# Kernel tuning notes

Measured on AMD Instinct MI355X. Metric: run time of the kernel, lower is better.

The kernel has to match this reference:

```python
import jax, jax.numpy as jnp
import numpy as np

NUM_HEADS = 16


def setup_inputs() -> dict:
    key = jax.random.key(0)
    k1, k2, k3 = jax.random.split(key, 3)
    x = jax.random.normal(k1, (2, 2048, 1024), dtype=jnp.float32)
    w_qkv = jax.random.normal(k2, (3072, 1024), dtype=jnp.float32) * 0.02
    b_qkv = jax.random.normal(k3, (3072,), dtype=jnp.float32) * 0.02
    return {"x": x, "w_qkv": w_qkv, "b_qkv": b_qkv}


def reference(x, w_qkv, b_qkv):
    b, s, _ = x.shape
    d_model = w_qkv.shape[0] // 3
    head_dim = d_model // NUM_HEADS
    # fused QKV projection (torch Linear: x @ W^T + b)
    qkv = x @ w_qkv.T + b_qkv                      # [b, s, 3*d_model]
    qkv = qkv.reshape(b, s, NUM_HEADS, 3 * head_dim)
    qkv = jnp.transpose(qkv, (0, 2, 1, 3))          # [b, h, s, 3*hd]
    q, k, v = jnp.split(qkv, 3, axis=-1)            # each [b, h, s, hd]
    scale = 1.0 / np.sqrt(head_dim).astype(np.float32)
    scores = jnp.einsum("bhqd,bhkd->bhqk", q, k) * scale
    attn = jax.nn.softmax(scores, axis=-1)
    values = jnp.einsum("bhqk,bhkd->bhqd", attn, v)  # [b, h, s, hd]
    # Faithful to source: reshape WITHOUT permuting heads back (head-interleaved)
    return values.reshape(b, s, d_model)
```

## Files before the change

### kernel.cpp

```cpp
#include <hip/hip_runtime.h>
#include <cstdint>

typedef unsigned short ushort_t;

#define M_ROWS 4096
#define N_COLS 3072
#define K_DIM  1024
#define S_LEN  2048
#define NHEADS 16
#define HDIM   64
#define QSCALE 0.1803368801111204f

typedef __bf16 bf16_t;
typedef bf16_t  bf16x8  __attribute__((ext_vector_type(8)));
typedef short   shortx4 __attribute__((ext_vector_type(4)));
typedef float   floatx4 __attribute__((ext_vector_type(4)));
typedef ushort_t ushortx4 __attribute__((ext_vector_type(4)));

union U32x2S4 { unsigned u[2]; shortx4 s; };

__device__ __forceinline__ unsigned short f2bf(float f) {
  unsigned u = __float_as_uint(f);
  u += 0x7FFFu + ((u >> 16) & 1u);
  return (unsigned short)(u >> 16);
}

__device__ __forceinline__ unsigned pkbf(float a, float b) {
  unsigned ua = __float_as_uint(a) + 0x8000u;
  unsigned ub = __float_as_uint(b) + 0x8000u;
  return __builtin_amdgcn_perm(ub, ua, 0x07060302u);
}

__device__ __forceinline__ unsigned cvtpk(float a, float b) {
#if __has_builtin(__builtin_amdgcn_cvt_pk_bf16_f32)
  auto t = __builtin_amdgcn_cvt_pk_bf16_f32(a, b);
  unsigned r;
  __builtin_memcpy(&r, &t, 4);
  return r;
#else
  return pkbf(a, b);
#endif
}

__device__ __forceinline__ float fexp2(float x) {
#if __has_builtin(__builtin_amdgcn_exp2f)
  return __builtin_amdgcn_exp2f(x);
#else
  float r; asm volatile("v_exp_f32 %0, %1\n\ts_nop 1" : "=v"(r) : "v"(x)); return r;
#endif
}

__device__ __forceinline__ void gload_lds16(const void* g, void* l) {
  __builtin_amdgcn_global_load_lds(
      (const __attribute__((address_space(1))) unsigned int*)g,
      (__attribute__((address_space(3))) unsigned int*)l,
      16, 0, 0);
}

__global__ __launch_bounds__(256) void cvt_bf16_kernel(
    const float* __restrict__ x, const float* __restrict__ w,
    ushort_t* __restrict__ Xb, ushort_t* __restrict__ Wb) {
  const int NX8 = (M_ROWS * K_DIM) / 8;
  int i = blockIdx.x * 256 + threadIdx.x;
  const float4* src;
  ushort_t* dst;
  int idx;
  if (i < NX8) { src = (const float4*)x; dst = Xb; idx = i; }
  else         { src = (const float4*)w; dst = Wb; idx = i - NX8; }
  float4 a = src[2 * idx];
  float4 b = src[2 * idx + 1];
  uint4 o;
  o.x = cvtpk(a.x, a.y);
  o.y = cvtpk(a.z, a.w);
  o.z = cvtpk(b.x, b.y);
  o.w = cvtpk(b.z, b.w);
  *(uint4*)(dst + 8 * (size_t)idx) = o;
}

__global__ __launch_bounds__(256) void qkv_gemm_kernel(
    const ushort_t* __restrict__ Xb, const ushort_t* __restrict__ Wb,
    const float* __restrict__ bias,
    ushort_t* __restrict__ Qb, ushort_t* __restrict__ Kb, ushort_t* __restrict__ Vb) {
  __shared__ ushort_t As[128 * 64];
  __shared__ ushort_t Bs[128 * 64];
  const int tid = threadIdx.x;
  const int l = tid & 63, w = tid >> 6;
  const int quad = l >> 4, lj = l & 15;
  const int m0 = blockIdx.y * 128, n0 = blockIdx.x * 128;
  const int wm = (w & 1) * 64, wn = (w >> 1) * 64;

  floatx4 acc[4][4] = {};

  const int srow = w * 32 + (l >> 3);
  const int scol = ((l & 7) ^ (l >> 3)) * 8;
  const ushort_t* gA = Xb + (size_t)(m0 + srow) * K_DIM + scol;
  const ushort_t* gB = Wb + (size_t)(n0 + srow) * K_DIM + scol;
  ushort_t* lA = As + (w * 32) * 64;
  ushort_t* lB = Bs + (w * 32) * 64;

  const int swr = lj & 7;

  for (int k0 = 0; k0 < K_DIM; k0 += 64) {
    __syncthreads();
#pragma unroll
    for (int c = 0; c < 4; ++c) {
      gload_lds16(gA + (size_t)(c * 8) * K_DIM + k0, lA + c * 8 * 64);
      gload_lds16(gB + (size_t)(c * 8) * K_DIM + k0, lB + c * 8 * 64);
    }
    __syncthreads();
#pragma unroll
    for (int kk = 0; kk < 2; ++kk) {
      const int ch = ((kk * 4 + quad) ^ swr) * 8;
      bf16x8 aF[4], bF[4];
#pragma unroll
      for (int i = 0; i < 4; ++i)
        aF[i] = *(const bf16x8*)(As + (wm + i * 16 + lj) * 64 + ch);
#pragma unroll
      for (int j = 0; j < 4; ++j)
        bF[j] = *(const bf16x8*)(Bs + (wn + j * 16 + lj) * 64 + ch);
#pragma unroll
      for (int i = 0; i < 4; ++i)
#pragma unroll
        for (int j = 0; j < 4; ++j)
          acc[i][j] = __builtin_amdgcn_mfma_f32_16x16x32_bf16(aF[i], bF[j], acc[i][j], 0, 0, 0);
    }
  }

#pragma unroll
  for (int j = 0; j < 4; ++j) {
    const int n = n0 + wn + j * 16 + lj;
    const int h = n / 192;
    const int r = n - h * 192;
    const int seg = r >> 6;
    const int d = r & 63;
    const float bv = bias[n];
    ushort_t* dst = (seg == 0) ? Qb : (seg == 1) ? Kb : Vb;
    const float scl = (seg == 0) ? QSCALE : 1.0f;
    const size_t base = (size_t)h * S_LEN * HDIM + d;
#pragma unroll
    for (int i = 0; i < 4; ++i) {
#pragma unroll
      for (int rg = 0; rg < 4; ++rg) {
        const int m = m0 + wm + i * 16 + quad * 4 + rg;
        const int bi = m >> 11;
        const int si = m & 2047;
        dst[base + ((size_t)bi * NHEADS * S_LEN + si) * HDIM] =
            f2bf((acc[i][j][rg] + bv) * scl);
      }
    }
  }
}

__global__ __launch_bounds__(512, 4) void attn_kernel(
    const ushort_t* __restrict__ Qb, const ushort_t* __restrict__ Kb,
    const ushort_t* __restrict__ Vb, float* __restrict__ out) {
  __shared__ ushort_t Ks[128 * 64];
  __shared__ ushort_t Vs[64 * 140];
  const int tid = threadIdx.x;
  const int l = tid & 63, w = tid >> 6;
  const int quad = l >> 4, lj = l & 15;
  const int bh = blockIdx.x >> 4;
  const int qt = blockIdx.x & 15;
  const int q0 = qt * 128 + w * 16;
  const size_t headoff = (size_t)bh * S_LEN * HDIM;

  bf16x8 qF[2];
#pragma unroll
  for (int kk = 0; kk < 2; ++kk)
    qF[kk] = *(const bf16x8*)(Qb + headoff + (size_t)(q0 + lj) * HDIM +
                              kk * 32 + quad * 8);

  floatx4 accO[4] = {};
  float l_runA = 0.f, l_runB = 0.f;

  const int kr = tid >> 3;
  const int kc = ((tid & 7) ^ (kr & 7)) * 8;
  const ushort_t* gK = Kb + headoff + (size_t)kr * HDIM + kc;
  ushort_t* lK = Ks + tid * 8;

  const int dq = tid & 15;
  const int spw = tid >> 4;
  const ushort_t* gV = Vb + headoff + dq * 4;
  unsigned* Vs32 = (unsigned*)Vs;
  const int swz = (dq >> 2) << 1;

  const int swk = lj & 7;

  for (int kb = 0; kb < 16; ++kb) {
    const int kv0 = kb * 128;
    __syncthreads();
#pragma unroll
    for (int c = 0; c < 2; ++c)
      gload_lds16(gK + (size_t)(kv0 + c * 64) * HDIM, lK + c * 64 * 64);
#pragma unroll
    for (int R = 0; R < 2; ++R) {
      const int sp = R * 32 + spw;
      const ushort_t* g = gV + (size_t)(kv0 + 2 * sp) * HDIM;
      const uint2 v0 = *(const uint2*)g;
      const uint2 v1 = *(const uint2*)(g + HDIM);
      unsigned o0 = __builtin_amdgcn_perm(v1.x, v0.x, 0x05040100u);
      unsigned o1 = __builtin_amdgcn_perm(v1.x, v0.x, 0x07060302u);
      unsigned o2 = __builtin_amdgcn_perm(v1.y, v0.y, 0x05040100u);
      unsigned o3 = __builtin_amdgcn_perm(v1.y, v0.y, 0x07060302u);
      const int sp2 = sp ^ swz;
      Vs32[(4 * dq + 0) * 70 + sp2] = o0;
      Vs32[(4 * dq + 1) * 70 + sp2] = o1;
      Vs32[(4 * dq + 2) * 70 + sp2] = o2;
      Vs32[(4 * dq + 3) * 70 + sp2] = o3;
    }
    __syncthreads();

    floatx4 accST[8];
#pragma unroll
    for (int c = 0; c < 8; ++c) {
      const ushort_t* krow = Ks + (c * 16 + lj) * 64;
      bf16x8 kF0 = *(const bf16x8*)(krow + ((quad ^ swk) * 8));
      bf16x8 kF1 = *(const bf16x8*)(krow + (((quad ^ swk) ^ 4) * 8));
      floatx4 z = {0.f, 0.f, 0.f, 0.f};
      z = __builtin_amdgcn_mfma_f32_16x16x32_bf16(kF0, qF[0], z, 0, 0, 0);
      accST[c] = __builtin_amdgcn_mfma_f32_16x16x32_bf16(kF1, qF[1], z, 0, 0, 0);
    }

    shortx4 aP[8];
    float lsA = 0.f, lsB = 0.f;
#pragma unroll
    for (int c = 0; c < 8; ++c) {
      float p0 = fexp2(accST[c][0]);
      float p1 = fexp2(accST[c][1]);
      float p2 = fexp2(accST[c][2]);
      float p3 = fexp2(accST[c][3]);
      lsA += p0 + p1;
      lsB += p2 + p3;
      U32x2S4 t;
      t.u[0] = cvtpk(p0, p1);
      t.u[1] = cvtpk(p2, p3);
      aP[c] = t.s;
    }
    l_runA += lsA;
    l_runB += lsB;

#pragma unroll
    for (int dt = 0; dt < 4; ++dt) {
      const ushort_t* vp = Vs + (dt * 16 + lj) * 140 + (quad ^ dt) * 4;
#pragma unroll
      for (int c = 0; c < 8; ++c) {
        shortx4 vF = *(const shortx4*)(vp + c * 16);
        accO[dt] = __builtin_amdgcn_mfma_f32_16x16x16bf16_1k(aP[c], vF, accO[dt], 0, 0, 0);
      }
    }
  }

  {
    float ls = l_runA + l_runB;
    ls += __shfl_xor(ls, 16, 64);
    ls += __shfl_xor(ls, 32, 64);
    const float inv = 1.0f / ls;
    const int sbase = (l & 48) | (quad * 4);
    float iv[4];
    iv[0] = __shfl(inv, sbase + 0, 64);
    iv[1] = __shfl(inv, sbase + 1, 64);
    iv[2] = __shfl(inv, sbase + 2, 64);
    iv[3] = __shfl(inv, sbase + 3, 64);
#pragma unroll
    for (int dt = 0; dt < 4; ++dt) {
#pragma unroll
      for (int rg = 0; rg < 4; ++rg) {
        const int q = q0 + quad * 4 + rg;
        out[headoff + (size_t)q * HDIM + dt * 16 + lj] = accO[dt][rg] * iv[rg];
      }
    }
  }
}

extern "C" void kernel_launch(void* const* d_in, const int* in_sizes, int n_in,
                              void* d_out, int out_size, void* d_ws, size_t ws_size,
                              hipStream_t stream) {
  (void)in_sizes; (void)n_in; (void)out_size; (void)ws_size;
  const float* x  = (const float*)d_in[0];
  const float* wq = (const float*)d_in[1];
  const float* bq = (const float*)d_in[2];
  float* out = (float*)d_out;

  char* ws = (char*)d_ws;
  ushort_t* Qb = (ushort_t*)(ws);
  ushort_t* Kb = (ushort_t*)(ws + 8388608);
  ushort_t* Vb = (ushort_t*)(ws + 16777216);
  ushort_t* Xb = (ushort_t*)(ws + 25165824);
  ushort_t* Wb = (ushort_t*)(ws + 33554432);

  cvt_bf16_kernel<<<3584, 256, 0, stream>>>(x, wq, Xb, Wb);
  qkv_gemm_kernel<<<dim3(N_COLS / 128, M_ROWS / 128), 256, 0, stream>>>(Xb, Wb, bq, Qb, Kb, Vb);
  attn_kernel<<<512, 512, 0, stream>>>(Qb, Kb, Vb, out);
}
```

Baseline: 158.9 us.

## Double-buffer K/V tiles in attention kernel to overlap loads with MFMA

The attention kernel now keeps two LDS buffers for K and V. The next tile's K is loaded asynchronously into LDS, and V is loaded into registers, while the current tile is being computed. The V transpose is written to LDS after the PV MFMAs, which leaves one barrier per iteration instead of two. The cost is doubled LDS use (about 68KB per block), which may limit occupancy below the launch_bounds target of 4 blocks, plus extra registers for the prefetched V.

```diff
diff --git a/kernel.cpp b/kernel.cpp
--- a/kernel.cpp
+++ b/kernel.cpp
@@ -154,8 +154,8 @@
 __global__ __launch_bounds__(512, 4) void attn_kernel(
     const ushort_t* __restrict__ Qb, const ushort_t* __restrict__ Kb,
     const ushort_t* __restrict__ Vb, float* __restrict__ out) {
-  __shared__ ushort_t Ks[128 * 64];
-  __shared__ ushort_t Vs[64 * 140];
+  __shared__ ushort_t Ks[2][128 * 64];
+  __shared__ ushort_t Vs[2][64 * 140];
   const int tid = threadIdx.x;
   const int l = tid & 63, w = tid >> 6;
   const int quad = l >> 4, lj = l & 15;
@@ -176,44 +176,59 @@
   const int kr = tid >> 3;
   const int kc = ((tid & 7) ^ (kr & 7)) * 8;
   const ushort_t* gK = Kb + headoff + (size_t)kr * HDIM + kc;
-  ushort_t* lK = Ks + tid * 8;
 
   const int dq = tid & 15;
   const int spw = tid >> 4;
   const ushort_t* gV = Vb + headoff + dq * 4;
-  unsigned* Vs32 = (unsigned*)Vs;
   const int swz = (dq >> 2) << 1;
 
   const int swk = lj & 7;
 
-  for (int kb = 0; kb < 16; ++kb) {
-    const int kv0 = kb * 128;
-    __syncthreads();
+  {
 #pragma unroll
     for (int c = 0; c < 2; ++c)
-      gload_lds16(gK + (size_t)(kv0 + c * 64) * HDIM, lK + c * 64 * 64);
+      gload_lds16(gK + (size_t)(c * 64) * HDIM, &Ks[0][tid * 8 + c * 64 * 64]);
+    unsigned* Vn = (unsigned*)Vs[0];
 #pragma unroll
     for (int R = 0; R < 2; ++R) {
       const int sp = R * 32 + spw;
-      const ushort_t* g = gV + (size_t)(kv0 + 2 * sp) * HDIM;
+      const ushort_t* g = gV + (size_t)(2 * sp) * HDIM;
       const uint2 v0 = *(const uint2*)g;
       const uint2 v1 = *(const uint2*)(g + HDIM);
-      unsigned o0 = __builtin_amdgcn_perm(v1.x, v0.x, 0x05040100u);
-      unsigned o1 = __builtin_amdgcn_perm(v1.x, v0.x, 0x07060302u);
-      unsigned o2 = __builtin_amdgcn_perm(v1.y, v0.y, 0x05040100u);
-      unsigned o3 = __builtin_amdgcn_perm(v1.y, v0.y, 0x07060302u);
       const int sp2 = sp ^ swz;
-      Vs32[(4 * dq + 0) * 70 + sp2] = o0;
-      Vs32[(4 * dq + 1) * 70 + sp2] = o1;
-      Vs32[(4 * dq + 2) * 70 + sp2] = o2;
-      Vs32[(4 * dq + 3) * 70 + sp2] = o3;
-    }
-    __syncthreads();
+      Vn[(4 * dq + 0) * 70 + sp2] = __builtin_amdgcn_perm(v1.x, v0.x, 0x05040100u);
+      Vn[(4 * dq + 1) * 70 + sp2] = __builtin_amdgcn_perm(v1.x, v0.x, 0x07060302u);
+      Vn[(4 * dq + 2) * 70 + sp2] = __builtin_amdgcn_perm(v1.y, v0.y, 0x05040100u);
+      Vn[(4 * dq + 3) * 70 + sp2] = __builtin_amdgcn_perm(v1.y, v0.y, 0x07060302u);
+    }
+  }
+  __syncthreads();
+
+#pragma unroll 2
+  for (int kb = 0; kb < 16; ++kb) {
+    const int cur = kb & 1;
+    const int nxt = cur ^ 1;
+
+    uint2 pv0[2], pv1[2];
+    if (kb < 15) {
+      const int kv1 = (kb + 1) * 128;
+#pragma unroll
+      for (int c = 0; c < 2; ++c)
+        gload_lds16(gK + (size_t)(kv1 + c * 64) * HDIM,
+                    &Ks[nxt][tid * 8 + c * 64 * 64]);
+#pragma unroll
+      for (int R = 0; R < 2; ++R) {
+        const int sp = R * 32 + spw;
+        const ushort_t* g = gV + (size_t)(kv1 + 2 * sp) * HDIM;
+        pv0[R] = *(const uint2*)g;
+        pv1[R] = *(const uint2*)(g + HDIM);
+      }
+    }
 
     floatx4 accST[8];
 #pragma unroll
     for (int c = 0; c < 8; ++c) {
-      const ushort_t* krow = Ks + (c * 16 + lj) * 64;
+      const ushort_t* krow = &Ks[cur][(c * 16 + lj) * 64];
       bf16x8 kF0 = *(const bf16x8*)(krow + ((quad ^ swk) * 8));
       bf16x8 kF1 = *(const bf16x8*)(krow + (((quad ^ swk) ^ 4) * 8));
       floatx4 z = {0.f, 0.f, 0.f, 0.f};
@@ -241,13 +256,27 @@
 
 #pragma unroll
     for (int dt = 0; dt < 4; ++dt) {
-      const ushort_t* vp = Vs + (dt * 16 + lj) * 140 + (quad ^ dt) * 4;
+      const ushort_t* vp = &Vs[cur][(dt * 16 + lj) * 140 + (quad ^ dt) * 4];
 #pragma unroll
       for (int c = 0; c < 8; ++c) {
         shortx4 vF = *(const shortx4*)(vp + c * 16);
         accO[dt] = __builtin_amdgcn_mfma_f32_16x16x16bf16_1k(aP[c], vF, accO[dt], 0, 0, 0);
       }
     }
+
+    if (kb < 15) {
+      unsigned* Vn = (unsigned*)Vs[nxt];
+#pragma unroll
+      for (int R = 0; R < 2; ++R) {
+        const int sp = R * 32 + spw;
+        const int sp2 = sp ^ swz;
+        Vn[(4 * dq + 0) * 70 + sp2] = __builtin_amdgcn_perm(pv1[R].x, pv0[R].x, 0x05040100u);
+        Vn[(4 * dq + 1) * 70 + sp2] = __builtin_amdgcn_perm(pv1[R].x, pv0[R].x, 0x07060302u);
+        Vn[(4 * dq + 2) * 70 + sp2] = __builtin_amdgcn_perm(pv1[R].y, pv0[R].y, 0x05040100u);
+        Vn[(4 * dq + 3) * 70 + sp2] = __builtin_amdgcn_perm(pv1[R].y, pv0[R].y, 0x07060302u);
+      }
+    }
+    __syncthreads();
   }
 
   {
```

Measured after the change: 172.7 us. 1.09x slower.
